# Optimization experiments

Measured on AMD Instinct MI355X. Metric: run time of the kernel, lower is better.

Reference implementation:

```python
import jax, jax.numpy as jnp
import numpy as np

MODEL_DIM = 2048
NUM_HEADS = 16
NUM_KV_HEADS = 4
HEAD_DIM = MODEL_DIM // NUM_HEADS  # 128
ROPE_BASE = 10000.0
LOCAL_WINDOW = 1024
EPS = 1.1920929e-07  # torch.finfo(float32).eps, F.rms_norm default
NEG = -1e30


def setup_inputs() -> dict:
    key = jax.random.key(0)
    ks = jax.random.split(key, 5)
    s = 0.02
    return {
        "x": jax.random.normal(ks[0], (1, 4096, MODEL_DIM), jnp.float32),
        "Wq": jax.random.normal(ks[1], (MODEL_DIM, MODEL_DIM), jnp.float32) * s,
        "Wk": jax.random.normal(ks[2], (NUM_KV_HEADS * HEAD_DIM, MODEL_DIM), jnp.float32) * s,
        "Wv": jax.random.normal(ks[3], (NUM_KV_HEADS * HEAD_DIM, MODEL_DIM), jnp.float32) * s,
        "Wo": jax.random.normal(ks[4], (MODEL_DIM, MODEL_DIM), jnp.float32) * s,
    }


def _rms_norm(x):
    return x * jax.lax.rsqrt(jnp.mean(x * x, axis=-1, keepdims=True) + EPS)


def _rope_tables(seqlen, dtype):
    inv_freq = 1.0 / (ROPE_BASE ** (jnp.arange(0, HEAD_DIM, 2, dtype=jnp.float32) / HEAD_DIM))
    freqs = jnp.arange(seqlen, dtype=jnp.float32)[:, None] * inv_freq[None, :]  # [S, hd/2]
    return jnp.cos(freqs).astype(dtype), jnp.sin(freqs).astype(dtype)


def _apply_rope(x, cos, sin):
    # x: [B, H, S, hd]; cos/sin: [S, hd/2]
    half = x.shape[-1] // 2
    x1, x2 = x[..., :half], x[..., half:]
    c = cos[None, None, :, :]
    s = sin[None, None, :, :]
    return jnp.concatenate((x1 * c + x2 * s, x2 * c - x1 * s), axis=-1)


def reference(x, Wq, Wk, Wv, Wo):
    B, S, _ = x.shape
    G = NUM_HEADS // NUM_KV_HEADS
    q = (x @ Wq.T).reshape(B, S, NUM_HEADS, HEAD_DIM).transpose(0, 2, 1, 3)
    k = (x @ Wk.T).reshape(B, S, NUM_KV_HEADS, HEAD_DIM).transpose(0, 2, 1, 3)
    v = (x @ Wv.T).reshape(B, S, NUM_KV_HEADS, HEAD_DIM).transpose(0, 2, 1, 3)
    q = _rms_norm(q)
    k = _rms_norm(k)
    cos, sin = _rope_tables(S, q.dtype)
    q = _apply_rope(q, cos, sin)
    k = _apply_rope(k, cos, sin)
    # GQA: expand kv heads to match query heads
    k = jnp.repeat(k, G, axis=1)  # [B, H, S, hd]
    v = jnp.repeat(v, G, axis=1)
    scale = 1.0 / np.sqrt(HEAD_DIM)
    scores = jnp.einsum("bhqd,bhkd->bhqk", q, k) * scale  # [B, H, S, S]
    idx = jnp.arange(S)
    causal = idx[None, :] <= idx[:, None]
    in_window = idx[None, :] > idx[:, None] - LOCAL_WINDOW
    allowed = causal & in_window  # [S, S]
    scores = jnp.where(allowed[None, None, :, :], scores, NEG)
    probs = jax.nn.softmax(scores, axis=-1)
    y = jnp.einsum("bhqk,bhkd->bhqd", probs, v)  # [B, H, S, hd]
    y = y.transpose(0, 2, 1, 3).reshape(B, S, MODEL_DIM)
    return y @ Wo.T
```

## Files before the change

kernel.cpp:

```cpp
#include <hip/hip_runtime.h>

typedef short bf16x8 __attribute__((ext_vector_type(8)));
typedef short short4v __attribute__((ext_vector_type(4)));
typedef float f32x4 __attribute__((ext_vector_type(4)));

__device__ __forceinline__ ushort f2b(float f) {
  union { float f; unsigned u; } v; v.f = f;
  unsigned r = v.u + 0x7FFF + ((v.u >> 16) & 1);
  return (ushort)(r >> 16);
}
__device__ __forceinline__ float b2f(ushort u) {
  union { unsigned u; float f; } v; v.u = ((unsigned)u) << 16;
  return v.f;
}
__device__ __forceinline__ unsigned cvtpk(float lo, float hi) {
  unsigned r;
  asm volatile("v_cvt_pk_bf16_f32 %0, %1, %2" : "=v"(r) : "v"(lo), "v"(hi));
  return r;
}
__device__ __forceinline__ f32x4 mfma16(bf16x8 a, bf16x8 b, f32x4 c) {
  return __builtin_amdgcn_mfma_f32_16x16x32_bf16(a, b, c, 0, 0, 0);
}

#define GLD_LDS16(g, l) \
  __builtin_amdgcn_global_load_lds((const __attribute__((address_space(1))) void*)(g), \
                                   (__attribute__((address_space(3))) void*)(l), 16, 0, 0)

__global__ __launch_bounds__(256) void cast_bf16(const float* __restrict__ in,
                                                 ushort* __restrict__ out, int n4) {
  int i = blockIdx.x * 256 + threadIdx.x;
  if (i >= n4) return;
  float4 f = ((const float4*)in)[i];
  ushort4 u;
  u.x = f2b(f.x); u.y = f2b(f.y); u.z = f2b(f.z); u.w = f2b(f.w);
  ((ushort4*)out)[i] = u;
}

__global__ void rope_tables_k(float* __restrict__ cosT, float* __restrict__ sinT) {
  int s = blockIdx.x, i = threadIdx.x;
  float inv = powf(10000.0f, -(float)i * (1.0f / 64.0f));
  float f = (float)s * inv;
  cosT[s * 64 + i] = cosf(f);
  sinT[s * 64 + i] = sinf(f);
}

template <bool BF16OUT>
__global__ __launch_bounds__(256) void gemm_bt(const ushort* __restrict__ A,
                                               const ushort* __restrict__ B,
                                               void* __restrict__ Cout,
                                               int M, int N, int K) {
  __shared__ __align__(16) ushort As[128 * 32];
  __shared__ __align__(16) ushort Bs[128 * 32];
  const int t = threadIdx.x;
  const int lane = t & 63, w = t >> 6;
  const int wr = w >> 1, wc = w & 1;
  const int l15 = lane & 15, l4 = lane >> 4;
  const long m0 = (long)blockIdx.y * 128, n0 = (long)blockIdx.x * 128;
  f32x4 acc[4][4] = {};
  const int srow = t >> 2, scol = (t & 3) * 8;
  const ushort* ga = A + (m0 + srow) * K + scol;
  const ushort* gb = B + (n0 + srow) * K + scol;
  for (int k0 = 0; k0 < K; k0 += 32) {
    GLD_LDS16(ga,          &As[t * 8]);
    GLD_LDS16(ga + 64 * K, &As[2048 + t * 8]);
    GLD_LDS16(gb,          &Bs[t * 8]);
    GLD_LDS16(gb + 64 * K, &Bs[2048 + t * 8]);
    ga += 32; gb += 32;
    asm volatile("s_waitcnt vmcnt(0)" ::: "memory");
    __syncthreads();
    bf16x8 af[4], bfr[4];
#pragma unroll
    for (int i = 0; i < 4; ++i) {
      af[i]  = *(const bf16x8*)(&As[(wr * 64 + i * 16 + l15) * 32 + l4 * 8]);
      bfr[i] = *(const bf16x8*)(&Bs[(wc * 64 + i * 16 + l15) * 32 + l4 * 8]);
    }
#pragma unroll
    for (int i = 0; i < 4; ++i)
#pragma unroll
      for (int j = 0; j < 4; ++j)
        acc[i][j] = mfma16(af[i], bfr[j], acc[i][j]);
    __syncthreads();
  }
#pragma unroll
  for (int i = 0; i < 4; ++i) {
#pragma unroll
    for (int j = 0; j < 4; ++j) {
      long mrow = m0 + wr * 64 + i * 16 + l4 * 4;
      long ncol = n0 + wc * 64 + j * 16 + l15;
#pragma unroll
      for (int r = 0; r < 4; ++r) {
        if constexpr (BF16OUT)
          ((ushort*)Cout)[(mrow + r) * N + ncol] = f2b(acc[i][j][r]);
        else
          ((float*)Cout)[(mrow + r) * N + ncol] = acc[i][j][r];
      }
    }
  }
}

__global__ __launch_bounds__(256) void postproc_k(const ushort* __restrict__ qkvb,
                                                  const float* __restrict__ cosT,
                                                  const float* __restrict__ sinT,
                                                  ushort* __restrict__ qb,
                                                  ushort* __restrict__ kb,
                                                  ushort* __restrict__ vtb) {
  const int lane = threadIdx.x & 63;
  const int s = blockIdx.x * 4 + (threadIdx.x >> 6);
  const int h = blockIdx.y;
  const int colbase = (h < 16) ? h * 128 : (h < 20 ? 2048 + (h - 16) * 128
                                                   : 2560 + (h - 20) * 128);
  const ushort* row = qkvb + (long)s * 3072 + colbase;
  float x1 = b2f(row[lane]), x2 = b2f(row[lane + 64]);
  if (h >= 20) {
    int kvh = h - 20;
    vtb[(long)(kvh * 128 + lane) * 4096 + s]      = f2b(x1);
    vtb[(long)(kvh * 128 + lane + 64) * 4096 + s] = f2b(x2);
    return;
  }
  float ss = x1 * x1 + x2 * x2;
#pragma unroll
  for (int m = 1; m < 64; m <<= 1) ss += __shfl_xor(ss, m);
  float rn = rsqrtf(ss * (1.0f / 128.0f) + 1.1920929e-07f);
  float c = cosT[s * 64 + lane], sn = sinT[s * 64 + lane];
  float x1n = x1 * rn, x2n = x2 * rn;
  float o1 = x1n * c + x2n * sn;
  float o2 = x2n * c - x1n * sn;
  if (h < 16) {
    const float scq = 0.08838834764831845f;
    ushort* dst = qb + ((long)h * 4096 + s) * 128;
    dst[lane] = f2b(o1 * scq);
    dst[lane + 64] = f2b(o2 * scq);
  } else {
    ushort* dst = kb + ((long)(h - 16) * 4096 + s) * 128;
    dst[lane] = f2b(o1);
    dst[lane + 64] = f2b(o2);
  }
}

__global__ __launch_bounds__(512) void attn_k(const ushort* __restrict__ qb,
                                              const ushort* __restrict__ kb,
                                              const ushort* __restrict__ vtb,
                                              ushort* __restrict__ yb) {
  __shared__ __align__(16) ushort lds[32768];
  const int t = threadIdx.x;
  const int lane = t & 63, w = t >> 6;
  const int l15 = lane & 15, l4 = lane >> 4;
  const int q0 = ((int)gridDim.x - 1 - (int)blockIdx.x) * 128;
  const int h = blockIdx.y, kvh = h >> 2;
  const int qw = q0 + w * 16;
  const int q = qw + l15;
  const int swz = l15 & 7;

  const ushort* Qp = qb + ((long)h * 4096 + q) * 128 + l4 * 8;
  bf16x8 qf[4];
#pragma unroll
  for (int c = 0; c < 4; ++c) qf[c] = *(const bf16x8*)(Qp + c * 32);

  const ushort* Kg = kb + (long)kvh * 4096 * 128;
  const ushort* Vg = vtb + (long)kvh * 128 * 4096;

  int kb_lo = q0 - 1023; if (kb_lo < 0) kb_lo = 0; kb_lo &= ~63;
  const int nt = (q0 + 127 - kb_lo) / 64 + 1;

  const int lbuA = (0 * 8 + w) * 512 + lane * 8;
  const int lbuB = (1 * 8 + w) * 512 + lane * 8;
  const int krA = lbuA >> 7, kcA = ((lbuA >> 3) & 15) ^ (krA & 7);
  const int krB = lbuB >> 7, kcB = ((lbuB >> 3) & 15) ^ (krB & 7);
  const int vrA = lbuA >> 6, vcA = ((lbuA >> 3) & 7) ^ (vrA & 7);
  const int vrB = lbuB >> 6, vcB = ((lbuB >> 3) & 7) ^ (vrB & 7);

#define STAGE(kbs, b)                                                        \
  do {                                                                       \
    ushort* Kl_ = &lds[(b) * 16384];                                         \
    ushort* Vl_ = &lds[(b) * 16384 + 8192];                                  \
    GLD_LDS16(Kg + (long)((kbs) + krA) * 128 + kcA * 8, Kl_ + lbuA);         \
    GLD_LDS16(Kg + (long)((kbs) + krB) * 128 + kcB * 8, Kl_ + lbuB);         \
    GLD_LDS16(Vg + (long)vrA * 4096 + (kbs) + vcA * 8, Vl_ + lbuA);          \
    GLD_LDS16(Vg + (long)vrB * 4096 + (kbs) + vcB * 8, Vl_ + lbuB);          \
  } while (0)

  f32x4 o[8] = {};
  float mrun = -1e30f, lrun = 0.0f;

  STAGE(kb_lo, 0);
  asm volatile("s_waitcnt vmcnt(0)" ::: "memory");
  __syncthreads();

  for (int ti = 0; ti < nt; ++ti) {
    const int kbs = kb_lo + ti * 64;
    const int cur = ti & 1;
    if (ti + 1 < nt) STAGE(kbs + 64, cur ^ 1);

    if (kbs + 63 >= qw - 1023 && kbs <= qw + 15) {
      const ushort* Kl = &lds[cur * 16384];
      const ushort* Vl = &lds[cur * 16384 + 8192];

      f32x4 sc[4];
#pragma unroll
      for (int st = 0; st < 4; ++st) {
        sc[st] = f32x4{0.f, 0.f, 0.f, 0.f};
        const ushort* kr = Kl + (st * 16 + l15) * 128;
#pragma unroll
        for (int c = 0; c < 4; ++c)
          sc[st] = mfma16(*(const bf16x8*)(kr + (((c * 4 + l4) ^ swz) * 8)), qf[c], sc[st]);
      }

      float s[16];
#pragma unroll
      for (int st = 0; st < 4; ++st)
#pragma unroll
        for (int r = 0; r < 4; ++r) {
          const int ki = kbs + st * 16 + l4 * 4 + r;
          s[st * 4 + r] = (ki <= q && ki > q - 1024) ? sc[st][r] : -1e30f;
        }

      float m0a = fmaxf(fmaxf(s[0], s[1]), fmaxf(s[2], s[3]));
      float m1a = fmaxf(fmaxf(s[4], s[5]), fmaxf(s[6], s[7]));
      float m2a = fmaxf(fmaxf(s[8], s[9]), fmaxf(s[10], s[11]));
      float m3a = fmaxf(fmaxf(s[12], s[13]), fmaxf(s[14], s[15]));
      float mx = fmaxf(fmaxf(m0a, m1a), fmaxf(m2a, m3a));
      mx = fmaxf(mx, __shfl_xor(mx, 16));
      mx = fmaxf(mx, __shfl_xor(mx, 32));

      float mn;
      if (__all(mx <= mrun + 8.0f)) {
        mn = mrun;
      } else {
        mn = fmaxf(mrun, mx);
        const float corr = __expf(mrun - mn);
        mrun = mn;
#pragma unroll
        for (int db = 0; db < 8; ++db)
#pragma unroll
          for (int r = 0; r < 4; ++r) o[db][r] *= corr;
        lrun *= corr;
      }

      float p[16];
#pragma unroll
      for (int j = 0; j < 16; ++j) p[j] = __expf(s[j] - mn);
      float ps = ((p[0] + p[1]) + (p[2] + p[3])) + ((p[4] + p[5]) + (p[6] + p[7]));
      ps += ((p[8] + p[9]) + (p[10] + p[11])) + ((p[12] + p[13]) + (p[14] + p[15]));
      ps += __shfl_xor(ps, 16);
      ps += __shfl_xor(ps, 32);
      lrun += ps;

      union { unsigned u[4]; bf16x8 v; } pa, pb;
      pa.u[0] = cvtpk(p[0], p[1]);   pa.u[1] = cvtpk(p[2], p[3]);
      pa.u[2] = cvtpk(p[4], p[5]);   pa.u[3] = cvtpk(p[6], p[7]);
      pb.u[0] = cvtpk(p[8], p[9]);   pb.u[1] = cvtpk(p[10], p[11]);
      pb.u[2] = cvtpk(p[12], p[13]); pb.u[3] = cvtpk(p[14], p[15]);

      const int co = 4 * (l4 & 1);
      const int c0 = (l4 >> 1) ^ swz, c1 = (2 + (l4 >> 1)) ^ swz;
      const int c2 = (4 + (l4 >> 1)) ^ swz, c3 = (6 + (l4 >> 1)) ^ swz;
#pragma unroll
      for (int db = 0; db < 8; ++db) {
        const ushort* vr = Vl + (db * 16 + l15) * 64;
        short4v a0 = *(const short4v*)(vr + c0 * 8 + co);
        short4v a1 = *(const short4v*)(vr + c1 * 8 + co);
        bf16x8 va = __builtin_shufflevector(a0, a1, 0, 1, 2, 3, 4, 5, 6, 7);
        o[db] = mfma16(va, pa.v, o[db]);
        short4v b0 = *(const short4v*)(vr + c2 * 8 + co);
        short4v b1 = *(const short4v*)(vr + c3 * 8 + co);
        bf16x8 vb = __builtin_shufflevector(b0, b1, 0, 1, 2, 3, 4, 5, 6, 7);
        o[db] = mfma16(vb, pb.v, o[db]);
      }
    }
    __syncthreads();
  }

  const float inv = 1.0f / lrun;
#pragma unroll
  for (int db = 0; db < 8; ++db)
#pragma unroll
    for (int r = 0; r < 4; ++r)
      yb[(long)q * 2048 + h * 128 + db * 16 + l4 * 4 + r] = f2b(o[db][r] * inv);
}

extern "C" void kernel_launch(void* const* d_in, const int* in_sizes, int n_in,
                              void* d_out, int out_size, void* d_ws, size_t ws_size,
                              hipStream_t stream) {
  (void)in_sizes; (void)n_in; (void)out_size; (void)ws_size;
  const float* x  = (const float*)d_in[0];
  const float* Wq = (const float*)d_in[1];
  const float* Wk = (const float*)d_in[2];
  const float* Wv = (const float*)d_in[3];
  const float* Wo = (const float*)d_in[4];
  const long S = 4096;
  ushort* ws   = (ushort*)d_ws;
  ushort* xb   = ws;
  ushort* wqkv = xb + S * 2048;
  ushort* wob  = wqkv + 3072L * 2048;
  ushort* qkvb = wob + 2048L * 2048;
  ushort* qb   = qkvb + S * 3072;
  ushort* kbuf = qb + S * 2048;
  ushort* vtb  = kbuf + 4L * 4096 * 128;
  ushort* yb   = vtb + 4L * 128 * 4096;
  float* cosT  = (float*)(yb + S * 2048);
  float* sinT  = cosT + S * 64;

  cast_bf16<<<dim3(8192), 256, 0, stream>>>(x, xb, (int)(S * 2048 / 4));
  cast_bf16<<<dim3(4096), 256, 0, stream>>>(Wq, wqkv, 2048 * 2048 / 4);
  cast_bf16<<<dim3(1024), 256, 0, stream>>>(Wk, wqkv + 2048L * 2048, 512 * 2048 / 4);
  cast_bf16<<<dim3(1024), 256, 0, stream>>>(Wv, wqkv + 2560L * 2048, 512 * 2048 / 4);
  cast_bf16<<<dim3(4096), 256, 0, stream>>>(Wo, wob, 2048 * 2048 / 4);

  gemm_bt<true><<<dim3(24, 32), 256, 0, stream>>>(xb, wqkv, qkvb, 4096, 3072, 2048);
  rope_tables_k<<<dim3(4096), 64, 0, stream>>>(cosT, sinT);
  postproc_k<<<dim3(1024, 24), 256, 0, stream>>>(qkvb, cosT, sinT, qb, kbuf, vtb);
  attn_k<<<dim3(32, 16), 512, 0, stream>>>(qb, kbuf, vtb, yb);
  gemm_bt<false><<<dim3(16, 32), 256, 0, stream>>>(yb, wob, d_out, 4096, 2048, 2048);
}
```

Baseline: 238.6 us.

## Replace GEMM with 256x128 tile, multi-stage LDS pipeline and swizzled layout

Rewrites the projection GEMM to use 512-thread blocks computing 256x128 tiles with K-step 64. A has a triple-buffered LDS ring and B a double-buffered one, with XOR-swizzled addresses. Loads for later K-steps are issued while MFMAs run on the current one, replacing the single-buffered load/wait/compute loop. This targets memory latency stalls and LDS bank conflicts. The cost is a 128KB LDS footprint per block, which limits occupancy, and fewer, larger blocks (384 and 256), which may underfill the CUs.

Measured after the change: 223.8 us. 6.2% less time.

```diff
diff --git a/kernel.cpp b/kernel.cpp
--- a/kernel.cpp
+++ b/kernel.cpp
@@ -45,57 +45,126 @@
 }
 
 template <bool BF16OUT>
-__global__ __launch_bounds__(256) void gemm_bt(const ushort* __restrict__ A,
+__global__ __launch_bounds__(512) void gemm256(const ushort* __restrict__ A,
                                                const ushort* __restrict__ B,
                                                void* __restrict__ Cout,
                                                int M, int N, int K) {
-  __shared__ __align__(16) ushort As[128 * 32];
-  __shared__ __align__(16) ushort Bs[128 * 32];
+  __shared__ __align__(16) ushort lds[65536];
   const int t = threadIdx.x;
   const int lane = t & 63, w = t >> 6;
-  const int wr = w >> 1, wc = w & 1;
+  const int wr = w & 3, wc = w >> 2;
   const int l15 = lane & 15, l4 = lane >> 4;
-  const long m0 = (long)blockIdx.y * 128, n0 = (long)blockIdx.x * 128;
+  const int nbn = N >> 7;
+  const long m0 = (long)(blockIdx.x / nbn) * 256;
+  const long n0 = (long)(blockIdx.x % nbn) * 128;
+  const int nk = K >> 6;
+
+  const int rd0 = l15 * 32 + l4 * 8;
+  const int rdoff = rd0 ^ ((((rd0 >> 6) & 3)) << 3);
+
+  int arow[4], acol[4], brow[2], bcol[2];
+#pragma unroll
+  for (int r = 0; r < 4; ++r) {
+    int us = r * 4096 + t * 8;
+    int uu = us ^ (((us >> 6) & 3) << 3);
+    int sub = uu >> 9;
+    arow[r] = (sub >> 1) * 16 + ((uu >> 5) & 15);
+    acol[r] = (sub & 1) * 32 + (uu & 31);
+    if (r < 2) { brow[r] = arow[r]; bcol[r] = acol[r]; }
+  }
+
+#define STAGE_A(kk, slot)                                                      \
+  do {                                                                         \
+    _Pragma("unroll") for (int r = 0; r < 4; ++r)                              \
+        GLD_LDS16(A + (m0 + arow[r]) * K + (kk) + acol[r],                     \
+                  &lds[(slot) * 16384 + r * 4096 + t * 8]);                    \
+  } while (0)
+#define STAGE_B(kk, slot)                                                      \
+  do {                                                                         \
+    _Pragma("unroll") for (int r = 0; r < 2; ++r)                              \
+        GLD_LDS16(B + (n0 + brow[r]) * K + (kk) + bcol[r],                     \
+                  &lds[49152 + (slot) * 8192 + r * 4096 + t * 8]);             \
+  } while (0)
+
   f32x4 acc[4][4] = {};
-  const int srow = t >> 2, scol = (t & 3) * 8;
-  const ushort* ga = A + (m0 + srow) * K + scol;
-  const ushort* gb = B + (n0 + srow) * K + scol;
-  for (int k0 = 0; k0 < K; k0 += 32) {
-    GLD_LDS16(ga,          &As[t * 8]);
-    GLD_LDS16(ga + 64 * K, &As[2048 + t * 8]);
-    GLD_LDS16(gb,          &Bs[t * 8]);
-    GLD_LDS16(gb + 64 * K, &Bs[2048 + t * 8]);
-    ga += 32; gb += 32;
-    asm volatile("s_waitcnt vmcnt(0)" ::: "memory");
-    __syncthreads();
-    bf16x8 af[4], bfr[4];
-#pragma unroll
-    for (int i = 0; i < 4; ++i) {
-      af[i]  = *(const bf16x8*)(&As[(wr * 64 + i * 16 + l15) * 32 + l4 * 8]);
-      bfr[i] = *(const bf16x8*)(&Bs[(wc * 64 + i * 16 + l15) * 32 + l4 * 8]);
+
+  STAGE_A(0, 0);
+  STAGE_B(0, 0);
+  STAGE_A(64, 1);
+
+  for (int j = 0; j < nk; ++j) {
+    const int sa = j % 3, sb = j & 1;
+    asm volatile("s_waitcnt vmcnt(4)" ::: "memory");
+    __builtin_amdgcn_s_barrier();
+
+    {
+      int kn = j + 1; if (kn > nk - 1) kn = nk - 1;
+      STAGE_B(kn * 64, (j + 1) & 1);
     }
-#pragma unroll
-    for (int i = 0; i < 4; ++i)
-#pragma unroll
-      for (int j = 0; j < 4; ++j)
-        acc[i][j] = mfma16(af[i], bfr[j], acc[i][j]);
-    __syncthreads();
-  }
+    bf16x8 bfrag[4][2], afrag[2][2];
+#pragma unroll
+    for (int n = 0; n < 4; ++n)
+#pragma unroll
+      for (int ks = 0; ks < 2; ++ks)
+        bfrag[n][ks] = *(const bf16x8*)(&lds[49152 + sb * 8192 +
+                                             ((wc * 4 + n) * 2 + ks) * 512 + rdoff]);
+#pragma unroll
+    for (int i = 0; i < 2; ++i)
+#pragma unroll
+      for (int ks = 0; ks < 2; ++ks)
+        afrag[i][ks] = *(const bf16x8*)(&lds[sa * 16384 +
+                                             ((wr * 4 + i) * 2 + ks) * 512 + rdoff]);
+    __builtin_amdgcn_s_setprio(1);
+#pragma unroll
+    for (int i = 0; i < 2; ++i)
+#pragma unroll
+      for (int n = 0; n < 4; ++n)
+#pragma unroll
+        for (int ks = 0; ks < 2; ++ks)
+          acc[i][n] = mfma16(afrag[i][ks], bfrag[n][ks], acc[i][n]);
+    __builtin_amdgcn_s_setprio(0);
+    __builtin_amdgcn_s_barrier();
+
+    {
+      int kn = j + 2; if (kn > nk - 1) kn = nk - 1;
+      STAGE_A(kn * 64, (j + 2) % 3);
+    }
+    bf16x8 afrag1[2][2];
+#pragma unroll
+    for (int i = 0; i < 2; ++i)
+#pragma unroll
+      for (int ks = 0; ks < 2; ++ks)
+        afrag1[i][ks] = *(const bf16x8*)(&lds[sa * 16384 +
+                                              ((wr * 4 + i + 2) * 2 + ks) * 512 + rdoff]);
+    __builtin_amdgcn_s_setprio(1);
+#pragma unroll
+    for (int i = 0; i < 2; ++i)
+#pragma unroll
+      for (int n = 0; n < 4; ++n)
+#pragma unroll
+        for (int ks = 0; ks < 2; ++ks)
+          acc[i + 2][n] = mfma16(afrag1[i][ks], bfrag[n][ks], acc[i + 2][n]);
+    __builtin_amdgcn_s_setprio(0);
+  }
+  asm volatile("s_waitcnt vmcnt(0)" ::: "memory");
+
 #pragma unroll
   for (int i = 0; i < 4; ++i) {
 #pragma unroll
-    for (int j = 0; j < 4; ++j) {
+    for (int n = 0; n < 4; ++n) {
       long mrow = m0 + wr * 64 + i * 16 + l4 * 4;
-      long ncol = n0 + wc * 64 + j * 16 + l15;
+      long ncol = n0 + wc * 64 + n * 16 + l15;
 #pragma unroll
       for (int r = 0; r < 4; ++r) {
         if constexpr (BF16OUT)
-          ((ushort*)Cout)[(mrow + r) * N + ncol] = f2b(acc[i][j][r]);
+          ((ushort*)Cout)[(mrow + r) * N + ncol] = f2b(acc[i][n][r]);
         else
-          ((float*)Cout)[(mrow + r) * N + ncol] = acc[i][j][r];
+          ((float*)Cout)[(mrow + r) * N + ncol] = acc[i][n][r];
       }
     }
   }
+#undef STAGE_A
+#undef STAGE_B
 }
 
 __global__ __launch_bounds__(256) void postproc_k(const ushort* __restrict__ qkvb,
@@ -306,9 +375,9 @@
   cast_bf16<<<dim3(1024), 256, 0, stream>>>(Wv, wqkv + 2560L * 2048, 512 * 2048 / 4);
   cast_bf16<<<dim3(4096), 256, 0, stream>>>(Wo, wob, 2048 * 2048 / 4);
 
-  gemm_bt<true><<<dim3(24, 32), 256, 0, stream>>>(xb, wqkv, qkvb, 4096, 3072, 2048);
+  gemm256<true><<<dim3(16 * 24), 512, 0, stream>>>(xb, wqkv, qkvb, 4096, 3072, 2048);
   rope_tables_k<<<dim3(4096), 64, 0, stream>>>(cosT, sinT);
   postproc_k<<<dim3(1024, 24), 256, 0, stream>>>(qkvb, cosT, sinT, qb, kbuf, vtb);
   attn_k<<<dim3(32, 16), 512, 0, stream>>>(qb, kbuf, vtb, yb);
-  gemm_bt<false><<<dim3(16, 32), 256, 0, stream>>>(yb, wob, d_out, 4096, 2048, 2048);
-}
+  gemm256<false><<<dim3(16 * 16), 512, 0, stream>>>(yb, wob, d_out, 4096, 2048, 2048);
+}
```
